# Kernel optimization log

Measured on AMD Instinct MI355X. Metric: run time of the kernel, lower is better.

Reference implementation:

```python
import jax, jax.numpy as jnp
import numpy as np

N_NODES = 100000
N_EDGES = 3200000
D = 128


def setup_inputs() -> dict:
    key = jax.random.key(0)
    k1, k2, k3, k4, k5 = jax.random.split(key, 5)
    x = jax.random.normal(k1, (N_NODES, D), dtype=jnp.float32)
    weight = jax.random.normal(k2, (D, D), dtype=jnp.float32) * (1.0 / np.sqrt(D))
    bias = jax.random.normal(k3, (D,), dtype=jnp.float32) * 0.01
    edge_weight = jax.random.uniform(k4, (N_EDGES,), dtype=jnp.float32)
    edge_index = jax.random.randint(k5, (2, N_EDGES), 0, N_NODES, dtype=jnp.int64 if jax.config.jax_enable_x64 else jnp.int32)
    return {"x": x, "weight": weight, "bias": bias,
            "edge_weight": edge_weight, "edge_index": edge_index}


def gcn_conv(x, weight, bias, edge_index, edge_weight):
    # PyG GCNConv defaults: normalize=True, add_self_loops=True (fill=1),
    # flow source_to_target: messages gathered from edge_index[0], scattered to edge_index[1].
    n = x.shape[0]
    src, dst = edge_index[0], edge_index[1]
    loop = jnp.arange(n, dtype=src.dtype)
    src = jnp.concatenate([src, loop])
    dst = jnp.concatenate([dst, loop])
    ew = jnp.concatenate([edge_weight, jnp.ones((n,), dtype=edge_weight.dtype)])
    deg = jax.ops.segment_sum(ew, dst, num_segments=n)          # [N]
    dinv = jnp.where(deg > 0, jax.lax.rsqrt(jnp.where(deg > 0, deg, 1.0)), 0.0)
    norm = dinv[src] * ew * dinv[dst]                           # [E+N]
    h = x @ weight.T                                            # [N, D_out]
    msg = h[src] * norm[:, None]                                # gather + scale
    out = jax.ops.segment_sum(msg, dst, num_segments=n)         # scatter-add
    return out + bias


def reference(x, weight, bias, edge_weight, edge_index):
    h = gcn_conv(x, weight, bias, edge_index, edge_weight)
    h = jax.nn.relu(h)            # normalizer is Identity, activation=F.relu
    h = h + x                     # input_dim == output_dim -> projection=Identity
    # dropout: eval mode (deterministic reference) -> no-op
    return h
```

## Files before the change

### kernel.cpp

```cpp
#include <hip/hip_runtime.h>

#define N_NODES 100000
#define N_EDGES 3200000
#define DIM 128

#define NB_C  98
#define CAP_C 36864
#define NB_F  1568
#define CAP_F 2560
#define CAP   96


typedef __attribute__((ext_vector_type(4))) float f32x4;
typedef __attribute__((ext_vector_type(8))) short s16x8;


__device__ __forceinline__ unsigned short f2bf(float f) {
    unsigned u = __float_as_uint(f);
    return (unsigned short)((u + 0x7fffu + ((u >> 16) & 1u)) >> 16);
}


__global__ __launch_bounds__(256) void zero_i_kernel(int* __restrict__ p, int n) {
    int i = blockIdx.x * 256 + threadIdx.x;
    if (i < n) p[i] = 0;
}

__global__ __launch_bounds__(256) void zero_f_kernel(float* __restrict__ p, int n) {
    int i = blockIdx.x * 256 + threadIdx.x;
    if (i < n) p[i] = 0.0f;
}

__global__ __launch_bounds__(256) void zero_u64_kernel(unsigned long long* __restrict__ p, int n) {
    int i = blockIdx.x * 256 + threadIdx.x;
    if (i < n) p[i] = 0ull;
}

__global__ __launch_bounds__(256) void zero_f4_kernel(float4* __restrict__ p, int n4) {
    int i = blockIdx.x * 256 + threadIdx.x;
    if (i < n4) p[i] = make_float4(0.f, 0.f, 0.f, 0.f);
}

__global__ __launch_bounds__(256) void dinv_kernel(float* __restrict__ deg) {
    int i = blockIdx.x * 256 + threadIdx.x;
    if (i < N_NODES) deg[i] = rsqrtf(deg[i] + 1.0f);
}

__global__ __launch_bounds__(256) void dinv_packed_kernel(const unsigned long long* __restrict__ packed,
                                                          float* __restrict__ dinv) {
    int i = blockIdx.x * 256 + threadIdx.x;
    if (i < N_NODES) {
        unsigned long long p = packed[i];
        float deg = (float)(p & 0xFFFFFFFFFFull) * (1.0f / 4294967296.0f);
        dinv[i] = rsqrtf(deg + 1.0f);
    }
}

__global__ __launch_bounds__(256) void wt_kernel(const float* __restrict__ W,
                                                 float* __restrict__ Wt) {
    int idx = blockIdx.x * 256 + threadIdx.x;
    int j = idx >> 7, k = idx & 127;
    Wt[k * 128 + j] = W[idx];
}


__global__ __launch_bounds__(256) void prep_kernel(const float* __restrict__ W,
                                                   ushort* __restrict__ wf_hi,
                                                   ushort* __restrict__ wf_lo,
                                                   int* __restrict__ fills) {
    const int b = blockIdx.x;
    const int tid = threadIdx.x;
    if (b < 64) {
        int idx  = b * 256 + tid;
        int j    = idx & 7;
        int lane = (idx >> 3) & 63;
        int ks   = (idx >> 9) & 3;
        int ct   = idx >> 11;
        int col  = ct * 16 + (lane & 15);
        int k    = ks * 32 + ((lane >> 4) << 3) + j;
        float w  = W[col * 128 + k];
        unsigned short hb = f2bf(w);
        float rem = w - __uint_as_float((unsigned)hb << 16);
        wf_hi[idx] = hb;
        wf_lo[idx] = f2bf(rem);
    } else {
        int i = (b - 64) * 256 + tid;
        if (i < NB_C + NB_F) fills[i] = 0;
    }
}


__global__ __launch_bounds__(256) void partA1_kernel(const int* __restrict__ ei,
                                                     const float* __restrict__ ew,
                                                     int* __restrict__ fill_c,
                                                     unsigned long long* __restrict__ edc) {
    __shared__ int hist[NB_C];
    __shared__ int base[NB_C];
    const int tid = threadIdx.x;
    const int blockbase = blockIdx.x * 4096;
    for (int i = tid; i < NB_C; i += 256) hist[i] = 0;
    __syncthreads();

    unsigned long long pay[16];
    unsigned meta[16];
#pragma unroll
    for (int i = 0; i < 16; ++i) {
        int e = blockbase + i * 256 + tid;
        meta[i] = 0xFFFFFFFFu;
        if (e < N_EDGES) {
            int src = ei[e];
            int dst = ei[N_EDGES + e];
            float w = ew[e];
            int cb = dst >> 10;
            int pos = atomicAdd(&hist[cb], 1);
            pay[i] = ((unsigned long long)__float_as_uint(w) << 32)
                   | ((unsigned)(dst & 1023) << 17) | (unsigned)src;
            meta[i] = ((unsigned)cb << 16) | (unsigned)pos;
        }
    }
    __syncthreads();
    for (int c = tid; c < NB_C; c += 256) {
        int cnt = hist[c];
        base[c] = (cnt > 0) ? atomicAdd(&fill_c[c], cnt) : 0;
    }
    __syncthreads();
#pragma unroll
    for (int i = 0; i < 16; ++i) {
        if (meta[i] != 0xFFFFFFFFu) {
            int cb = (int)(meta[i] >> 16);
            int pos = base[cb] + (int)(meta[i] & 0xFFFFu);
            if (pos < CAP_C)
                edc[(unsigned)cb * CAP_C + (unsigned)pos] = pay[i];
        }
    }
}


__global__ __launch_bounds__(256) void partA2_kernel(const int* __restrict__ fill_c,
                                                     const unsigned long long* __restrict__ edc,
                                                     int* __restrict__ fill_f,
                                                     unsigned long long* __restrict__ edf) {
    __shared__ int hist[16];
    __shared__ int base[16];
    const int tid = threadIdx.x;
    const int cb = blockIdx.x / 9;
    const int lo = (blockIdx.x % 9) * 4096;
    const int cnt_c = min(fill_c[cb], CAP_C);
    const int hi = min(lo + 4096, cnt_c);
    if (tid < 16) hist[tid] = 0;
    __syncthreads();

    unsigned long long pay[16];
    unsigned meta[16];
#pragma unroll
    for (int i = 0; i < 16; ++i) {
        int idx = lo + i * 256 + tid;
        meta[i] = 0xFFFFFFFFu;
        if (idx < hi) {
            unsigned long long p = edc[(unsigned)cb * CAP_C + (unsigned)idx];
            int f = (int)((p >> 23) & 15);
            int pos = atomicAdd(&hist[f], 1);
            pay[i] = p;
            meta[i] = ((unsigned)f << 16) | (unsigned)pos;
        }
    }
    __syncthreads();
    if (tid < 16) {
        int c = hist[tid];
        base[tid] = (c > 0) ? atomicAdd(&fill_f[cb * 16 + tid], c) : 0;
    }
    __syncthreads();
#pragma unroll
    for (int i = 0; i < 16; ++i) {
        if (meta[i] != 0xFFFFFFFFu) {
            int f = (int)(meta[i] >> 16);
            int pos = base[f] + (int)(meta[i] & 0xFFFFu);
            if (pos < CAP_F)
                edf[((unsigned)(cb * 16 + f)) * CAP_F + (unsigned)pos] = pay[i];
        }
    }
}


__global__ __launch_bounds__(256) void partB_kernel(const int* __restrict__ fill_f,
                                                    unsigned long long* __restrict__ edf,
                                                    float* __restrict__ dinv,
                                                    int* __restrict__ row_start,
                                                    int* __restrict__ row_cnt,
                                                    const float4* __restrict__ x4,
                                                    ushort4* __restrict__ xh4) {
    __shared__ int hist[64];
    __shared__ float degs[64];
    __shared__ int pref[64];
    const int tid = threadIdx.x;
    const int fb = blockIdx.x;
    const int node_base = fb * 64;
    const int cnt = min(fill_f[fb], CAP_F);
    if (tid < 64) { hist[tid] = 0; degs[tid] = 0.0f; }
    __syncthreads();

    unsigned long long pay[10];
    unsigned meta[10];
    int m = 0;
    for (int idx = tid; idx < cnt; idx += 256) {
        unsigned long long p = edf[(unsigned)fb * CAP_F + (unsigned)idx];
        int dl = (int)((p >> 17) & 63);
        int pos = atomicAdd(&hist[dl], 1);
        atomicAdd(&degs[dl], __uint_as_float((unsigned)(p >> 32)));
        pay[m] = p;
        meta[m] = ((unsigned)dl << 16) | (unsigned)pos;
        ++m;
    }
    __syncthreads();
    if (tid == 0) {
        int run = 0;
#pragma unroll
        for (int n = 0; n < 64; ++n) { pref[n] = run; run += hist[n]; }
    }
    __syncthreads();
    if (tid < 64) {
        int node = node_base + tid;
        if (node < N_NODES) {
            float dv = rsqrtf(degs[tid] + 1.0f);
            dinv[node] = dv;
            degs[tid] = dv;
            row_start[node] = fb * CAP_F + pref[tid];
            row_cnt[node] = hist[tid];
        }
    }
    for (int i = 0; i < m; ++i) {
        int dl = (int)(meta[i] >> 16);
        edf[(unsigned)fb * CAP_F + (unsigned)(pref[dl] + (int)(meta[i] & 0xFFFFu))] = pay[i];
    }
    __syncthreads();
#pragma unroll
    for (int i = 0; i < 8; ++i) {
        int idx = i * 256 + tid;
        int r = idx >> 5;
        int node = node_base + r;
        if (node < N_NODES) {
            float dv = degs[r];
            float4 v = x4[(unsigned)node * 32u + (unsigned)(idx & 31)];
            ushort4 h;
            h.x = f2bf(v.x * dv); h.y = f2bf(v.y * dv);
            h.z = f2bf(v.z * dv); h.w = f2bf(v.w * dv);
            xh4[(unsigned)node * 32u + (unsigned)(idx & 31)] = h;
        }
    }
}


__global__ __launch_bounds__(256) void gatherc_kernel(const int* __restrict__ row_start,
                                                      const int* __restrict__ row_cnt,
                                                      const unsigned long long* __restrict__ edf,
                                                      const float* __restrict__ dinv,
                                                      const unsigned* __restrict__ xh,
                                                      float2* __restrict__ agg2) {
    const int lane = threadIdx.x & 63;
    const int node = blockIdx.x * 4 + (threadIdx.x >> 6);

    const int cnt = row_cnt[node];
    const int start = row_start[node];
    float ax0 = 0.f, ay0 = 0.f, ax1 = 0.f, ay1 = 0.f;

    for (int b = 0; b < cnt; b += 64) {
        int idx = b + lane;
        const bool valid = idx < cnt;
        if (!valid) idx = cnt - 1;
        unsigned long long p = edf[(unsigned)(start + idx)];
        int msrc = (int)(p & 0x1FFFFull);
        float mw = valid ? __uint_as_float((unsigned)(p >> 32)) : 0.0f;
        const int mcnt = min(64, cnt - b);
        const int ng = (mcnt + 7) >> 3;

        unsigned va[8], vb[8];

#define PREF(buf, JB)                                                          \
        _Pragma("unroll")                                                      \
        for (int j = 0; j < 8; ++j) {                                          \
            int s = __builtin_amdgcn_readlane(msrc, (JB) + j);                 \
            buf[j] = xh[(unsigned)s * 64u + (unsigned)lane];                   \
        }
#define CONSUME(buf, JB)                                                       \
        _Pragma("unroll")                                                      \
        for (int j = 0; j < 8; ++j) {                                          \
            float w = __int_as_float(                                          \
                __builtin_amdgcn_readlane(__float_as_int(mw), (JB) + j));      \
            if (j & 1) {                                                       \
                ax1 = fmaf(__uint_as_float(buf[j] << 16), w, ax1);             \
                ay1 = fmaf(__uint_as_float(buf[j] & 0xffff0000u), w, ay1);     \
            } else {                                                           \
                ax0 = fmaf(__uint_as_float(buf[j] << 16), w, ax0);             \
                ay0 = fmaf(__uint_as_float(buf[j] & 0xffff0000u), w, ay0);     \
            }                                                                  \
        }

        PREF(va, 0);
        int g = 0;
        for (; g + 2 < ng; g += 2) {
            PREF(vb, (g + 1) * 8);
            CONSUME(va, g * 8);
            PREF(va, (g + 2) * 8);
            CONSUME(vb, (g + 1) * 8);
        }
        if (g + 1 < ng) {
            PREF(vb, (g + 1) * 8);
            CONSUME(va, g * 8);
            CONSUME(vb, (g + 1) * 8);
        } else {
            CONSUME(va, g * 8);
        }
#undef PREF
#undef CONSUME
    }

    float di = dinv[node];
    agg2[(unsigned)node * 64u + lane] = make_float2((ax0 + ax1) * di, (ay0 + ay1) * di);
}


__global__ __launch_bounds__(256) void bucket_f32_kernel(const int* __restrict__ ei,
                                                         const float* __restrict__ ew,
                                                         unsigned long long* __restrict__ packed,
                                                         int2* __restrict__ ed) {
    int e = blockIdx.x * 256 + threadIdx.x;
    int src = ei[e];
    int dst = ei[N_EDGES + e];
    float w = ew[e];
    unsigned long long inc = (1ull << 40) | (unsigned long long)(w * 4294967296.0f);
    unsigned long long old = atomicAdd(&packed[dst], inc);
    unsigned slot = (unsigned)(old >> 40);
    if (slot < CAP) {
        ed[(unsigned)dst * CAP + slot] = make_int2(src, __float_as_int(w));
    }
}

__global__ __launch_bounds__(256) void gatherb_f32_kernel(const unsigned long long* __restrict__ packed,
                                                          const int2* __restrict__ ed,
                                                          const float* __restrict__ dinv,
                                                          const float2* __restrict__ x2,
                                                          float2* __restrict__ agg2) {
    const int wave = threadIdx.x >> 6;
    const int lane = threadIdx.x & 63;
    const int node = blockIdx.x * 4 + wave;

    int cnt = (int)(packed[node] >> 40);
    cnt = min(cnt, CAP);
    const unsigned base = (unsigned)node * CAP;
    float2 acc = make_float2(0.f, 0.f);

    for (int b = 0; b < cnt; b += 64) {
        int idx = b + lane;
        if (idx >= cnt) idx = cnt - 1;
        int2 my = ed[base + idx];
        float wmy = __int_as_float(my.y) * dinv[my.x];
        int m = min(64, cnt - b);
#pragma unroll 8
        for (int j = 0; j < m; ++j) {
            int s = __builtin_amdgcn_readlane(my.x, j);
            float w = __int_as_float(__builtin_amdgcn_readlane(__float_as_int(wmy), j));
            float2 v = x2[(unsigned)s * 64u + lane];
            acc.x = fmaf(v.x, w, acc.x); acc.y = fmaf(v.y, w, acc.y);
        }
    }
    float di = dinv[node];
    acc.x *= di; acc.y *= di;
    agg2[(unsigned)node * 64u + lane] = acc;
}

__global__ __launch_bounds__(256) void count_deg_kernel(const int* __restrict__ ei,
                                                        const float* __restrict__ ew,
                                                        int* __restrict__ count,
                                                        float* __restrict__ deg) {
    int e = blockIdx.x * 256 + threadIdx.x;
    int dst = ei[N_EDGES + e];
    atomicAdd(&count[dst], 1);
    atomicAdd(&deg[dst], ew[e]);
}

__global__ __launch_bounds__(256) void scatter_kernel(const int* __restrict__ ei,
                                                      const float* __restrict__ ew,
                                                      const float* __restrict__ dinv,
                                                      const float4* __restrict__ x4,
                                                      float* __restrict__ agg) {
    unsigned gid = blockIdx.x * 256u + threadIdx.x;
    unsigned e  = gid >> 5;
    unsigned f4 = gid & 31u;
    int src = ei[e];
    int dst = ei[N_EDGES + e];
    float w = dinv[src] * ew[e] * dinv[dst];
    float4 v = x4[(unsigned)src * 32u + f4];
    float* o = agg + ((unsigned)dst * 128u + f4 * 4u);
    atomicAdd(o + 0, v.x * w);
    atomicAdd(o + 1, v.y * w);
    atomicAdd(o + 2, v.z * w);
    atomicAdd(o + 3, v.w * w);
}


__global__ __launch_bounds__(256) void final_mfma_kernel(const float* __restrict__ agg_in,
                                                         const float* __restrict__ x,
                                                         const float* __restrict__ bias,
                                                         const float* __restrict__ dinv,
                                                         const ushort* __restrict__ wf_hi,
                                                         const ushort* __restrict__ wf_lo,
                                                         float* __restrict__ out) {
    __shared__ ushort sh_hi[16384];
    __shared__ ushort sh_lo[16384];
    const int tid = threadIdx.x;
    {
        const float4* sh4 = (const float4*)wf_hi;
        const float4* sl4 = (const float4*)wf_lo;
        float4* dh = (float4*)sh_hi;
        float4* dl = (float4*)sh_lo;
#pragma unroll
        for (int i = 0; i < 8; ++i) {
            dh[i * 256 + tid] = sh4[i * 256 + tid];
            dl[i * 256 + tid] = sl4[i * 256 + tid];
        }
    }
    __syncthreads();

    const int wave = tid >> 6;
    const int lane = tid & 63;
    const int r0 = blockIdx.x * 64 + wave * 16;
    const int mrow = lane & 15;
    const int kg = lane >> 4;
    const int arow = min(r0 + mrow, N_NODES - 1);
    const float di = dinv[arow];
    const float di2 = di * di;

    s16x8 ah[4], al[4];
#pragma unroll
    for (int ks = 0; ks < 4; ++ks) {
        const float* ap = agg_in + (unsigned)arow * 128u + ks * 32 + kg * 8;
        const float* xp = x      + (unsigned)arow * 128u + ks * 32 + kg * 8;
        float4 a0 = *(const float4*)ap;
        float4 a1 = *(const float4*)(ap + 4);
        float4 x0 = *(const float4*)xp;
        float4 x1 = *(const float4*)(xp + 4);
        float v[8] = {a0.x + x0.x * di2, a0.y + x0.y * di2,
                      a0.z + x0.z * di2, a0.w + x0.w * di2,
                      a1.x + x1.x * di2, a1.y + x1.y * di2,
                      a1.z + x1.z * di2, a1.w + x1.w * di2};
        s16x8 h, l;
#pragma unroll
        for (int j = 0; j < 8; ++j) {
            unsigned short hb = f2bf(v[j]);
            h[j] = (short)hb;
            l[j] = (short)f2bf(v[j] - __uint_as_float((unsigned)hb << 16));
        }
        ah[ks] = h; al[ks] = l;
    }

#pragma unroll
    for (int ct = 0; ct < 8; ++ct) {
        f32x4 acc = {0.f, 0.f, 0.f, 0.f};
#pragma unroll
        for (int ks = 0; ks < 4; ++ks) {
            const int fo = ((ct * 4 + ks) * 64 + lane) * 8;
            s16x8 bh = *(const s16x8*)&sh_hi[fo];
            s16x8 bl = *(const s16x8*)&sh_lo[fo];
            acc = __builtin_amdgcn_mfma_f32_16x16x32_bf16(ah[ks], bh, acc, 0, 0, 0);
            acc = __builtin_amdgcn_mfma_f32_16x16x32_bf16(ah[ks], bl, acc, 0, 0, 0);
            acc = __builtin_amdgcn_mfma_f32_16x16x32_bf16(al[ks], bh, acc, 0, 0, 0);
        }
        const int col = ct * 16 + mrow;
        const float bv = bias[col];
#pragma unroll
        for (int v = 0; v < 4; ++v) {
            const int row = r0 + kg * 4 + v;
            if (row < N_NODES) {
                float o = fmaxf(acc[v] + bv, 0.f) + x[(unsigned)row * 128u + col];
                out[(unsigned)row * 128u + col] = o;
            }
        }
    }
}


__global__ __launch_bounds__(256) void final_kernel(const float* __restrict__ agg_in,
                                                    const float* __restrict__ x,
                                                    const float* __restrict__ bias,
                                                    const float* __restrict__ dinv,
                                                    const float* __restrict__ Wt,
                                                    float* __restrict__ out) {
    __shared__ float sh_wt[16384];
    const int tid = threadIdx.x;
    {
        const float4* s4 = (const float4*)Wt;
        float4* d4 = (float4*)sh_wt;
#pragma unroll
        for (int i = 0; i < 16; ++i) d4[i * 256 + tid] = s4[i * 256 + tid];
    }
    __syncthreads();

    const int wave = tid >> 6;
    const int lane = tid & 63;
    const int rowbase = blockIdx.x * 32 + wave * 8;

    float areg[16];
#pragma unroll
    for (int r = 0; r < 8; ++r) {
        int row = rowbase + r;
        float di = dinv[row];
        float di2 = di * di;
        int base = row * 128;
        areg[2 * r]     = agg_in[base + lane]      + x[base + lane]      * di2;
        areg[2 * r + 1] = agg_in[base + 64 + lane] + x[base + 64 + lane] * di2;
    }

    float acc0[8], acc1[8];
#pragma unroll
    for (int r = 0; r < 8; ++r) { acc0[r] = 0.f; acc1[r] = 0.f; }

    const float2* wt2 = (const float2*)sh_wt;

#pragma unroll
    for (int kh = 0; kh < 2; ++kh) {
#pragma unroll 16
        for (int kk = 0; kk < 64; ++kk) {
            int k = kh * 64 + kk;
            float2 w = wt2[k * 64 + lane];
#pragma unroll
            for (int r = 0; r < 8; ++r) {
                float ak = __uint_as_float(
                    __builtin_amdgcn_readlane(__float_as_uint(areg[2 * r + kh]), kk));
                acc0[r] = fmaf(ak, w.x, acc0[r]);
                acc1[r] = fmaf(ak, w.y, acc1[r]);
            }
        }
    }

    float2 b = ((const float2*)bias)[lane];
#pragma unroll
    for (int r = 0; r < 8; ++r) {
        int row = rowbase + r;
        float2 xr = ((const float2*)x)[row * 64 + lane];
        float v0 = fmaxf(acc0[r] + b.x, 0.f) + xr.x;
        float v1 = fmaxf(acc1[r] + b.y, 0.f) + xr.y;
        ((float2*)out)[row * 64 + lane] = make_float2(v0, v1);
    }
}


extern "C" void kernel_launch(void* const* d_in, const int* in_sizes, int n_in,
                              void* d_out, int out_size, void* d_ws, size_t ws_size,
                              hipStream_t stream) {
    const float* x    = (const float*)d_in[0];
    const float* W    = (const float*)d_in[1];
    const float* bias = (const float*)d_in[2];
    const float* ew   = (const float*)d_in[3];
    const int*   ei   = (const int*)d_in[4];
    float* out = (float*)d_out;
    char* ws = (char*)d_ws;

    unsigned short* xhA  = (unsigned short*)ws;
    ushort* wfhi     = (ushort*)(ws + 25600000);
    ushort* wflo     = wfhi + 16384;
    float* dinvA     = (float*)(ws + 25665536);
    int*   row_start = (int*)  (ws + 26065536);
    int*   row_cnt   = (int*)  (ws + 26465536);
    int*   fill_c    = (int*)  (ws + 26865536);
    int*   fill_f    = fill_c + NB_C;
    unsigned long long* edc = (unsigned long long*)(ws + 26872256);
    unsigned long long* edf = (unsigned long long*)(ws + 55773632);
    const size_t WS_PART = 87886272ull;

    unsigned long long* packed = (unsigned long long*)ws;
    float* dinvB = (float*)(ws + 800000);
    float* WtB   = (float*)(ws + 1200000);
    int2*  edB   = (int2*)(ws + 1265536);
    const size_t WS_BUCKET = 1265536ull + (size_t)N_NODES * CAP * 8ull;

    if (ws_size >= WS_PART) {
        prep_kernel<<<71, 256, 0, stream>>>(W, wfhi, wflo, fill_c);
        partA1_kernel<<<(N_EDGES + 4095) / 4096, 256, 0, stream>>>(ei, ew, fill_c, edc);
        partA2_kernel<<<NB_C * 9, 256, 0, stream>>>(fill_c, edc, fill_f, edf);
        partB_kernel<<<NB_F, 256, 0, stream>>>(fill_f, edf, dinvA, row_start, row_cnt,
                                               (const float4*)x, (ushort4*)xhA);
        gatherc_kernel<<<N_NODES / 4, 256, 0, stream>>>(row_start, row_cnt, edf, dinvA,
                                                        (const unsigned*)xhA, (float2*)out);
        final_mfma_kernel<<<(N_NODES + 63) / 64, 256, 0, stream>>>(out, x, bias, dinvA,
                                                                   wfhi, wflo, out);
    } else if (ws_size >= WS_BUCKET) {
        zero_u64_kernel<<<(N_NODES + 255) / 256, 256, 0, stream>>>(packed, N_NODES);
        wt_kernel<<<64, 256, 0, stream>>>(W, WtB);
        bucket_f32_kernel<<<N_EDGES / 256, 256, 0, stream>>>(ei, ew, packed, edB);
        dinv_packed_kernel<<<(N_NODES + 255) / 256, 256, 0, stream>>>(packed, dinvB);
        gatherb_f32_kernel<<<N_NODES / 4, 256, 0, stream>>>(packed, edB, dinvB,
                                                            (const float2*)x, (float2*)out);
        final_kernel<<<N_NODES / 32, 256, 0, stream>>>(out, x, bias, dinvB, WtB, out);
    } else {
        float* deg   = (float*)(ws);
        float* Wt    = (float*)(ws + 400000);
        int*   count = (int*)  (ws + 465536);
        zero_f_kernel<<<(N_NODES + 255) / 256, 256, 0, stream>>>(deg, N_NODES);
        zero_i_kernel<<<(N_NODES + 255) / 256, 256, 0, stream>>>(count, N_NODES);
        wt_kernel<<<64, 256, 0, stream>>>(W, Wt);
        zero_f4_kernel<<<(N_NODES * DIM / 4) / 256, 256, 0, stream>>>((float4*)out,
                                                                      N_NODES * DIM / 4);
        count_deg_kernel<<<N_EDGES / 256, 256, 0, stream>>>(ei, ew, count, deg);
        dinv_kernel<<<(N_NODES + 255) / 256, 256, 0, stream>>>(deg);
        scatter_kernel<<<(N_EDGES / 256) * 32, 256, 0, stream>>>(ei, ew, deg,
                                                                 (const float4*)x, out);
        final_kernel<<<N_NODES / 32, 256, 0, stream>>>(out, x, bias, deg, Wt, out);
    }
}
```

Baseline: 362.2 us.

## Fuse CSR gather aggregation with MFMA linear layer and epilogue

Merges the gather kernel and the final MFMA kernel into one. Each wave aggregates 16 destination nodes one at a time and adds the self-loop term. It then splits the result into bf16 hi/lo, stages it in swizzled shared memory, and runs the split-bf16 MFMA with bias, ReLU and residual directly. This removes the fp32 write and re-read of the aggregated [N,128] intermediate and one kernel launch. In exchange it loses parallelism: 1568 blocks each walk 16 nodes serially per wave instead of one node per wave, and weights are now read from global/L2 rather than LDS.

```diff
diff --git a/kernel.cpp b/kernel.cpp
--- a/kernel.cpp
+++ b/kernel.cpp
@@ -250,72 +250,130 @@
 }
 
 
-__global__ __launch_bounds__(256) void gatherc_kernel(const int* __restrict__ row_start,
+__global__ __launch_bounds__(256) void gatherf_kernel(const int* __restrict__ row_start,
                                                       const int* __restrict__ row_cnt,
                                                       const unsigned long long* __restrict__ edf,
                                                       const float* __restrict__ dinv,
                                                       const unsigned* __restrict__ xh,
-                                                      float2* __restrict__ agg2) {
-    const int lane = threadIdx.x & 63;
-    const int node = blockIdx.x * 4 + (threadIdx.x >> 6);
-
-    const int cnt = row_cnt[node];
-    const int start = row_start[node];
-    float ax0 = 0.f, ay0 = 0.f, ax1 = 0.f, ay1 = 0.f;
-
-    for (int b = 0; b < cnt; b += 64) {
-        int idx = b + lane;
-        const bool valid = idx < cnt;
-        if (!valid) idx = cnt - 1;
-        unsigned long long p = edf[(unsigned)(start + idx)];
-        int msrc = (int)(p & 0x1FFFFull);
-        float mw = valid ? __uint_as_float((unsigned)(p >> 32)) : 0.0f;
-        const int mcnt = min(64, cnt - b);
-        const int ng = (mcnt + 7) >> 3;
-
-        unsigned va[8], vb[8];
+                                                      const float2* __restrict__ x2,
+                                                      const ushort* __restrict__ wf_hi,
+                                                      const ushort* __restrict__ wf_lo,
+                                                      const float* __restrict__ bias,
+                                                      const float* __restrict__ x,
+                                                      float* __restrict__ out) {
+    __shared__ unsigned shA_hi[4][1024];
+    __shared__ unsigned shA_lo[4][1024];
+    const int tid = threadIdx.x;
+    const int wave = tid >> 6;
+    const int lane = tid & 63;
+    const int nb = blockIdx.x * 64 + wave * 16;
+
+    for (int i = 0; i < 16; ++i) {
+        const int node = nb + i;
+        const bool live = node < N_NODES;
+        const int cnt = live ? row_cnt[node] : 0;
+        const int start = live ? row_start[node] : 0;
+        const float di = live ? dinv[node] : 0.0f;
+        float ax0 = 0.f, ay0 = 0.f, ax1 = 0.f, ay1 = 0.f;
+
+        for (int b = 0; b < cnt; b += 64) {
+            int idx = b + lane;
+            const bool valid = idx < cnt;
+            if (!valid) idx = cnt - 1;
+            unsigned long long p = edf[(unsigned)(start + idx)];
+            int msrc = (int)(p & 0x1FFFFull);
+            float mw = valid ? __uint_as_float((unsigned)(p >> 32)) : 0.0f;
+            const int mcnt = min(64, cnt - b);
+            const int ng = (mcnt + 7) >> 3;
+
+            unsigned va[8], vb[8];
 
 #define PREF(buf, JB)                                                          \
-        _Pragma("unroll")                                                      \
-        for (int j = 0; j < 8; ++j) {                                          \
-            int s = __builtin_amdgcn_readlane(msrc, (JB) + j);                 \
-            buf[j] = xh[(unsigned)s * 64u + (unsigned)lane];                   \
-        }
+            _Pragma("unroll")                                                  \
+            for (int j = 0; j < 8; ++j) {                                      \
+                int s = __builtin_amdgcn_readlane(msrc, (JB) + j);             \
+                buf[j] = xh[(unsigned)s * 64u + (unsigned)lane];               \
+            }
 #define CONSUME(buf, JB)                                                       \
-        _Pragma("unroll")                                                      \
-        for (int j = 0; j < 8; ++j) {                                          \
-            float w = __int_as_float(                                          \
-                __builtin_amdgcn_readlane(__float_as_int(mw), (JB) + j));      \
-            if (j & 1) {                                                       \
-                ax1 = fmaf(__uint_as_float(buf[j] << 16), w, ax1);             \
-                ay1 = fmaf(__uint_as_float(buf[j] & 0xffff0000u), w, ay1);     \
-            } else {                                                           \
-                ax0 = fmaf(__uint_as_float(buf[j] << 16), w, ax0);             \
-                ay0 = fmaf(__uint_as_float(buf[j] & 0xffff0000u), w, ay0);     \
-            }                                                                  \
-        }
-
-        PREF(va, 0);
-        int g = 0;
-        for (; g + 2 < ng; g += 2) {
-            PREF(vb, (g + 1) * 8);
-            CONSUME(va, g * 8);
-            PREF(va, (g + 2) * 8);
-            CONSUME(vb, (g + 1) * 8);
-        }
-        if (g + 1 < ng) {
-            PREF(vb, (g + 1) * 8);
-            CONSUME(va, g * 8);
-            CONSUME(vb, (g + 1) * 8);
-        } else {
-            CONSUME(va, g * 8);
-        }
+            _Pragma("unroll")                                                  \
+            for (int j = 0; j < 8; ++j) {                                      \
+                float w = __int_as_float(                                      \
+                    __builtin_amdgcn_readlane(__float_as_int(mw), (JB) + j));  \
+                if (j & 1) {                                                   \
+                    ax1 = fmaf(__uint_as_float(buf[j] << 16), w, ax1);         \
+                    ay1 = fmaf(__uint_as_float(buf[j] & 0xffff0000u), w, ay1); \
+                } else {                                                       \
+                    ax0 = fmaf(__uint_as_float(buf[j] << 16), w, ax0);         \
+                    ay0 = fmaf(__uint_as_float(buf[j] & 0xffff0000u), w, ay0); \
+                }                                                              \
+            }
+
+            PREF(va, 0);
+            int g = 0;
+            for (; g + 2 < ng; g += 2) {
+                PREF(vb, (g + 1) * 8);
+                CONSUME(va, g * 8);
+                PREF(va, (g + 2) * 8);
+                CONSUME(vb, (g + 1) * 8);
+            }
+            if (g + 1 < ng) {
+                PREF(vb, (g + 1) * 8);
+                CONSUME(va, g * 8);
+                CONSUME(vb, (g + 1) * 8);
+            } else {
+                CONSUME(va, g * 8);
+            }
 #undef PREF
 #undef CONSUME
-    }
-
-    float di = dinv[node];
-    agg2[(unsigned)node * 64u + lane] = make_float2((ax0 + ax1) * di, (ay0 + ay1) * di);
+        }
+
+        const float di2 = di * di;
+        float2 xr = x2[(unsigned)(live ? node : 0) * 64u + lane];
+        float a0 = (ax0 + ax1) * di + xr.x * di2;
+        float a1 = (ay0 + ay1) * di + xr.y * di2;
+        unsigned h0 = f2bf(a0);
+        unsigned l0 = f2bf(a0 - __uint_as_float(h0 << 16));
+        unsigned h1 = f2bf(a1);
+        unsigned l1 = f2bf(a1 - __uint_as_float(h1 << 16));
+        unsigned w = (unsigned)(i * 64 + lane) ^ ((unsigned)(i & 7) << 2);
+        shA_hi[wave][w] = h0 | (h1 << 16);
+        shA_lo[wave][w] = l0 | (l1 << 16);
+    }
+    __syncthreads();
+
+    const int mrow = lane & 15;
+    const int kg = lane >> 4;
+    s16x8 ah[4], al[4];
+#pragma unroll
+    for (int ks = 0; ks < 4; ++ks) {
+        unsigned w = (unsigned)(mrow * 64 + ks * 16 + kg * 4) ^ ((unsigned)(mrow & 7) << 2);
+        ah[ks] = *(const s16x8*)&shA_hi[wave][w];
+        al[ks] = *(const s16x8*)&shA_lo[wave][w];
+    }
+
+#pragma unroll
+    for (int ct = 0; ct < 8; ++ct) {
+        f32x4 acc = {0.f, 0.f, 0.f, 0.f};
+#pragma unroll
+        for (int ks = 0; ks < 4; ++ks) {
+            const int fo = ((ct * 4 + ks) * 64 + lane) * 8;
+            s16x8 bh = *(const s16x8*)&wf_hi[fo];
+            s16x8 bl = *(const s16x8*)&wf_lo[fo];
+            acc = __builtin_amdgcn_mfma_f32_16x16x32_bf16(ah[ks], bh, acc, 0, 0, 0);
+            acc = __builtin_amdgcn_mfma_f32_16x16x32_bf16(ah[ks], bl, acc, 0, 0, 0);
+            acc = __builtin_amdgcn_mfma_f32_16x16x32_bf16(al[ks], bh, acc, 0, 0, 0);
+        }
+        const int col = ct * 16 + mrow;
+        const float bv = bias[col];
+#pragma unroll
+        for (int v = 0; v < 4; ++v) {
+            const int row = nb + kg * 4 + v;
+            if (row < N_NODES) {
+                float o = fmaxf(acc[v] + bv, 0.f) + x[(unsigned)row * 128u + col];
+                out[(unsigned)row * 128u + col] = o;
+            }
+        }
+    }
 }
 
 
@@ -398,87 +456,6 @@
 }
 
 
-__global__ __launch_bounds__(256) void final_mfma_kernel(const float* __restrict__ agg_in,
-                                                         const float* __restrict__ x,
-                                                         const float* __restrict__ bias,
-                                                         const float* __restrict__ dinv,
-                                                         const ushort* __restrict__ wf_hi,
-                                                         const ushort* __restrict__ wf_lo,
-                                                         float* __restrict__ out) {
-    __shared__ ushort sh_hi[16384];
-    __shared__ ushort sh_lo[16384];
-    const int tid = threadIdx.x;
-    {
-        const float4* sh4 = (const float4*)wf_hi;
-        const float4* sl4 = (const float4*)wf_lo;
-        float4* dh = (float4*)sh_hi;
-        float4* dl = (float4*)sh_lo;
-#pragma unroll
-        for (int i = 0; i < 8; ++i) {
-            dh[i * 256 + tid] = sh4[i * 256 + tid];
-            dl[i * 256 + tid] = sl4[i * 256 + tid];
-        }
-    }
-    __syncthreads();
-
-    const int wave = tid >> 6;
-    const int lane = tid & 63;
-    const int r0 = blockIdx.x * 64 + wave * 16;
-    const int mrow = lane & 15;
-    const int kg = lane >> 4;
-    const int arow = min(r0 + mrow, N_NODES - 1);
-    const float di = dinv[arow];
-    const float di2 = di * di;
-
-    s16x8 ah[4], al[4];
-#pragma unroll
-    for (int ks = 0; ks < 4; ++ks) {
-        const float* ap = agg_in + (unsigned)arow * 128u + ks * 32 + kg * 8;
-        const float* xp = x      + (unsigned)arow * 128u + ks * 32 + kg * 8;
-        float4 a0 = *(const float4*)ap;
-        float4 a1 = *(const float4*)(ap + 4);
-        float4 x0 = *(const float4*)xp;
-        float4 x1 = *(const float4*)(xp + 4);
-        float v[8] = {a0.x + x0.x * di2, a0.y + x0.y * di2,
-                      a0.z + x0.z * di2, a0.w + x0.w * di2,
-                      a1.x + x1.x * di2, a1.y + x1.y * di2,
-                      a1.z + x1.z * di2, a1.w + x1.w * di2};
-        s16x8 h, l;
-#pragma unroll
-        for (int j = 0; j < 8; ++j) {
-            unsigned short hb = f2bf(v[j]);
-            h[j] = (short)hb;
-            l[j] = (short)f2bf(v[j] - __uint_as_float((unsigned)hb << 16));
-        }
-        ah[ks] = h; al[ks] = l;
-    }
-
-#pragma unroll
-    for (int ct = 0; ct < 8; ++ct) {
-        f32x4 acc = {0.f, 0.f, 0.f, 0.f};
-#pragma unroll
-        for (int ks = 0; ks < 4; ++ks) {
-            const int fo = ((ct * 4 + ks) * 64 + lane) * 8;
-            s16x8 bh = *(const s16x8*)&sh_hi[fo];
-            s16x8 bl = *(const s16x8*)&sh_lo[fo];
-            acc = __builtin_amdgcn_mfma_f32_16x16x32_bf16(ah[ks], bh, acc, 0, 0, 0);
-            acc = __builtin_amdgcn_mfma_f32_16x16x32_bf16(ah[ks], bl, acc, 0, 0, 0);
-            acc = __builtin_amdgcn_mfma_f32_16x16x32_bf16(al[ks], bh, acc, 0, 0, 0);
-        }
-        const int col = ct * 16 + mrow;
-        const float bv = bias[col];
-#pragma unroll
-        for (int v = 0; v < 4; ++v) {
-            const int row = r0 + kg * 4 + v;
-            if (row < N_NODES) {
-                float o = fmaxf(acc[v] + bv, 0.f) + x[(unsigned)row * 128u + col];
-                out[(unsigned)row * 128u + col] = o;
-            }
-        }
-    }
-}
-
-
 __global__ __launch_bounds__(256) void final_kernel(const float* __restrict__ agg_in,
                                                     const float* __restrict__ x,
                                                     const float* __restrict__ bias,
@@ -579,18 +556,18 @@
         partA2_kernel<<<NB_C * 9, 256, 0, stream>>>(fill_c, edc, fill_f, edf);
         partB_kernel<<<NB_F, 256, 0, stream>>>(fill_f, edf, dinvA, row_start, row_cnt,
                                                (const float4*)x, (ushort4*)xhA);
-        gatherc_kernel<<<N_NODES / 4, 256, 0, stream>>>(row_start, row_cnt, edf, dinvA,
-                                                        (const unsigned*)xhA, (float2*)out);
-        final_mfma_kernel<<<(N_NODES + 63) / 64, 256, 0, stream>>>(out, x, bias, dinvA,
-                                                                   wfhi, wflo, out);
+        gatherf_kernel<<<NB_F, 256, 0, stream>>>(row_start, row_cnt, edf, dinvA,
+                                                 (const unsigned*)xhA, (const float2*)x,
+                                                 wfhi, wflo, bias, x, out);
     } else if (ws_size >= WS_BUCKET) {
+        float* WtB_f = WtB;
         zero_u64_kernel<<<(N_NODES + 255) / 256, 256, 0, stream>>>(packed, N_NODES);
-        wt_kernel<<<64, 256, 0, stream>>>(W, WtB);
+        wt_kernel<<<64, 256, 0, stream>>>(W, WtB_f);
         bucket_f32_kernel<<<N_EDGES / 256, 256, 0, stream>>>(ei, ew, packed, edB);
         dinv_packed_kernel<<<(N_NODES + 255) / 256, 256, 0, stream>>>(packed, dinvB);
         gatherb_f32_kernel<<<N_NODES / 4, 256, 0, stream>>>(packed, edB, dinvB,
                                                             (const float2*)x, (float2*)out);
-        final_kernel<<<N_NODES / 32, 256, 0, stream>>>(out, x, bias, dinvB, WtB, out);
+        final_kernel<<<N_NODES / 32, 256, 0, stream>>>(out, x, bias, dinvB, WtB_f, out);
     } else {
         float* deg   = (float*)(ws);
         float* Wt    = (float*)(ws + 400000);
```

Result: slower. 370.2 us (+2.2%).
